# Performance work log

Measured on AMD Instinct MI355X. Metric: run time of the kernel, lower is better.

Reference implementation:

```python
import jax, jax.numpy as jnp
import numpy as np

MAX_SHIFT = 2
SMOOTH = 1.0

def setup_inputs() -> dict:
    key = jax.random.key(0)
    k1, k2 = jax.random.split(key)
    # predicted probabilities in [0,1)
    inputs = jax.random.uniform(k1, (64, 1, 512, 512), dtype=jnp.float32)
    # soft targets (the original accepts any float mask); uniform works as a stand-in
    targets = jax.random.uniform(k2, (64, 1, 512, 512), dtype=jnp.float32)
    return {"inputs": inputs, "targets": targets}

def reference(inputs, targets):
    # all (shift_y, shift_x) pairs from the 5x5 nested loop
    shifts = jnp.array(
        [(sy, sx)
         for sx in range(-MAX_SHIFT, MAX_SHIFT + 1)
         for sy in range(-MAX_SHIFT, MAX_SHIFT + 1)],
        dtype=jnp.int32,
    )  # [25, 2]

    # global sums; targets.sum() is invariant under roll but kept per the original math
    i_sum = inputs.sum()
    t_sum = targets.sum()

    def dice_loss(shift):
        st = jnp.roll(targets, (shift[0], shift[1]), axis=(2, 3))
        intersection = jnp.sum(inputs * st)
        return 1.0 - (2.0 * intersection + SMOOTH) / (i_sum + t_sum + SMOOTH)

    losses = jax.vmap(dice_loss)(shifts)  # [25]
    return jnp.min(losses)
```

## Files before the change

### kernel.cpp

```cpp
#include <hip/hip_runtime.h>

#define H 512
#define W 512
#define RROWS 32
#define TGR  (RROWS + 4)
#define NCHUNK (TGR * 2)

__device__ __forceinline__ float wave_sum_dpp(float x) {
#define DPP_STEP(ctrl)                                                          \
    x += __int_as_float(__builtin_amdgcn_update_dpp(                            \
        0, __float_as_int(x), (ctrl), 0xF, 0xF, true))
    DPP_STEP(0x111);
    DPP_STEP(0x112);
    DPP_STEP(0x114);
    DPP_STEP(0x118);
    DPP_STEP(0x142);
    DPP_STEP(0x143);
#undef DPP_STEP
    return x;
}

__device__ __forceinline__ float4 ld4(const float* p) {
    return *reinterpret_cast<const float4*>(p);
}
__device__ __forceinline__ float2 ld2(const float* p) {
    return *reinterpret_cast<const float2*>(p);
}

__device__ __forceinline__ void gl_lds16(const float* g, float* l) {
    __builtin_amdgcn_global_load_lds(
        (const __attribute__((address_space(1))) void*)g,
        (__attribute__((address_space(3))) void*)l,
        16, 0, 0);
}

__global__ __launch_bounds__(512, 4)
void dice_partial(const float* __restrict__ in, const float* __restrict__ tg,
                  float* __restrict__ ws, int nblocks) {
    __shared__ __align__(16) float tgs[TGR * W];
    __shared__ float warr[8][32];

    const int tid  = threadIdx.x;
    const int wave = tid >> 6, lane = tid & 63;

    const int bid = blockIdx.x;
    const int wrk = (bid & 7) * (nblocks >> 3) + (bid >> 3);

    const int b  = wrk >> 4;
    const int y0 = (wrk & 15) * RROWS;
    const float* __restrict__ ib = in + (size_t)b * (H * W);
    const float* __restrict__ tb = tg + (size_t)b * (H * W);

    const int c0 = lane * 8;

    const int ry = y0 + wave * 4;
    float4 ia[4], ic[4];
#pragma unroll
    for (int yi = 0; yi < 4; ++yi) {
        const float* rp = ib + (size_t)(ry + yi) * W;
        ia[yi] = ld4(rp + c0);
        ic[yi] = ld4(rp + c0 + 4);
    }

#pragma unroll
    for (int k = 0; k < 9; ++k) {
        const int c    = wave * 9 + k;
        const int rr   = c >> 1;
        const int half = (c & 1) * 256;
        const int ra   = (y0 - 2 + rr) & (H - 1);
        gl_lds16(tb + (size_t)ra * W + half + lane * 4, &tgs[c * 256]);
    }

    float iv[4][8];
    float isum = 0.f;
#pragma unroll
    for (int yi = 0; yi < 4; ++yi) {
        iv[yi][0] = ia[yi].x; iv[yi][1] = ia[yi].y;
        iv[yi][2] = ia[yi].z; iv[yi][3] = ia[yi].w;
        iv[yi][4] = ic[yi].x; iv[yi][5] = ic[yi].y;
        iv[yi][6] = ic[yi].z; iv[yi][7] = ic[yi].w;
#pragma unroll
        for (int j = 0; j < 8; ++j) isum += iv[yi][j];
    }
    isum = wave_sum_dpp(isum);
    if (lane == 63) warr[wave][25] = isum;

    __syncthreads();

    float acc[25];
#pragma unroll
    for (int k = 0; k < 25; ++k) acc[k] = 0.f;
    float tsum = 0.f;

#pragma unroll
    for (int t = 0; t < 8; ++t) {
        const float* rowp = &tgs[(wave * 4 + t) * W];
        float tw[12];
        const float4 a  = ld4(rowp + c0);
        const float4 cc = ld4(rowp + c0 + 4);
        const float2 lf = ld2(rowp + ((c0 - 2) & (W - 1)));
        const float2 rg = ld2(rowp + ((c0 + 8) & (W - 1)));
        tw[0]  = lf.x; tw[1]  = lf.y;
        tw[2]  = a.x;  tw[3]  = a.y;  tw[4] = a.z;  tw[5] = a.w;
        tw[6]  = cc.x; tw[7]  = cc.y; tw[8] = cc.z; tw[9] = cc.w;
        tw[10] = rg.x; tw[11] = rg.y;

        if (t >= 2 && t <= 5) {
#pragma unroll
            for (int j = 0; j < 8; ++j) tsum += tw[j + 2];
        }

#pragma unroll
        for (int yi = 0; yi < 4; ++yi) {
            const int sy = yi + 2 - t;
            if (sy < -2 || sy > 2) continue;
#pragma unroll
            for (int sx = -2; sx <= 2; ++sx) {
#pragma unroll
                for (int j = 0; j < 8; ++j)
                    acc[(sy + 2) * 5 + (sx + 2)] += iv[yi][j] * tw[j + 2 - sx];
            }
        }
    }

#pragma unroll
    for (int k = 0; k < 25; ++k) {
        const float v = wave_sum_dpp(acc[k]);
        if (lane == 63) warr[wave][k] = v;
    }
    {
        const float u = wave_sum_dpp(tsum);
        if (lane == 63) warr[wave][26] = u;
    }

    __syncthreads();
    if (tid < 27) {
        float s = 0.f;
#pragma unroll
        for (int w = 0; w < 8; ++w) s += warr[w][tid];
        ws[tid * nblocks + bid] = s;
    }
}

__global__ __launch_bounds__(256)
void dice_reduce(const float* __restrict__ ws, float* __restrict__ tot, int nblocks) {
    __shared__ float red[4];
    const int k = blockIdx.x;
    const int tid = threadIdx.x;
    const float* p = ws + (size_t)k * nblocks;

    float s = 0.f;
    for (int i = tid; i < nblocks; i += 256) s += p[i];
    s = wave_sum_dpp(s);
    if ((tid & 63) == 63) red[tid >> 6] = s;
    __syncthreads();
    if (tid == 0) tot[k] = red[0] + red[1] + red[2] + red[3];
}

__global__ void dice_out(const float* __restrict__ tot, float* __restrict__ out) {
    const int tid = threadIdx.x;
    float v = (tid < 25) ? tot[tid] : -1e30f;
#pragma unroll
    for (int off = 32; off; off >>= 1) v = fmaxf(v, __shfl_down(v, off, 64));
    if (tid == 0) {
        const float denom = tot[25] + tot[26] + 1.0f;
        out[0] = 1.0f - (2.0f * v + 1.0f) / denom;
    }
}

extern "C" void kernel_launch(void* const* d_in, const int* in_sizes, int n_in,
                              void* d_out, int out_size, void* d_ws, size_t ws_size,
                              hipStream_t stream) {
    const float* inputs  = (const float*)d_in[0];
    const float* targets = (const float*)d_in[1];
    float* out = (float*)d_out;
    float* ws  = (float*)d_ws;

    const int B = in_sizes[0] / (H * W);
    const int nblocks = B * (H / RROWS);

    float* tot = ws + (size_t)27 * nblocks;

    dice_partial<<<nblocks, 512, 0, stream>>>(inputs, targets, ws, nblocks);
    dice_reduce<<<27, 256, 0, stream>>>(ws, tot, nblocks);
    dice_out<<<1, 64, 0, stream>>>(tot, out);
}
```

Before: 38.76 us.

## Double-buffer slabs of inputs and targets in LDS with async loads

Each block now handles 64 rows of one image, split into 8 slabs of 8 rows. For each slab, both the input rows and the haloed target rows are staged into double-buffered LDS with global_load_lds, and the next slab's load is issued while the current one is computed. This overlaps memory traffic with the 25-shift correlation work, and the target halo is reloaded once per 8 rows instead of once per 32. The cost is more halo re-reads of targets, smaller 256-thread blocks, a barrier per slab, and only 512 blocks in the grid, which may lower parallelism and occupancy.

```diff
diff --git a/kernel.cpp b/kernel.cpp
--- a/kernel.cpp
+++ b/kernel.cpp
@@ -2,9 +2,10 @@
 
 #define H 512
 #define W 512
-#define RROWS 32
-#define TGR  (RROWS + 4)
-#define NCHUNK (TGR * 2)
+#define SLAB 8
+#define TROWS 12
+#define BROWS 20
+#define NSLAB 8
 
 __device__ __forceinline__ float wave_sum_dpp(float x) {
 #define DPP_STEP(ctrl)                                                          \
@@ -34,11 +35,10 @@
         16, 0, 0);
 }
 
-__global__ __launch_bounds__(512, 4)
+__global__ __launch_bounds__(256)
 void dice_partial(const float* __restrict__ in, const float* __restrict__ tg,
                   float* __restrict__ ws, int nblocks) {
-    __shared__ __align__(16) float tgs[TGR * W];
-    __shared__ float warr[8][32];
+    __shared__ __align__(16) float buf[2][BROWS][W];
 
     const int tid  = threadIdx.x;
     const int wave = tid >> 6, lane = tid & 63;
@@ -46,98 +46,103 @@
     const int bid = blockIdx.x;
     const int wrk = (bid & 7) * (nblocks >> 3) + (bid >> 3);
 
-    const int b  = wrk >> 4;
-    const int y0 = (wrk & 15) * RROWS;
-    const float* __restrict__ ib = in + (size_t)b * (H * W);
-    const float* __restrict__ tb = tg + (size_t)b * (H * W);
+    const int b   = wrk >> 3;
+    const int r0  = (wrk & 7) * 64;
+    const float* __restrict__ inb = in + (size_t)b * (H * W);
+    const float* __restrict__ tgb = tg + (size_t)b * (H * W);
 
     const int c0 = lane * 8;
 
-    const int ry = y0 + wave * 4;
-    float4 ia[4], ic[4];
-#pragma unroll
-    for (int yi = 0; yi < 4; ++yi) {
-        const float* rp = ib + (size_t)(ry + yi) * W;
-        ia[yi] = ld4(rp + c0);
-        ic[yi] = ld4(rp + c0 + 4);
+#define STAGE(s, sb) {                                                          \
+        const int y0s = r0 + (s) * SLAB;                                        \
+        _Pragma("unroll")                                                       \
+        for (int k = 0; k < 10; ++k) {                                          \
+            const int e    = wave * 10 + k;                                     \
+            const int rr   = e >> 1;                                            \
+            const int half = (e & 1) * 256;                                     \
+            const float* src = (rr < TROWS)                                     \
+                ? tgb + (size_t)((y0s - 2 + rr) & (H - 1)) * W + half           \
+                : inb + (size_t)(y0s + (rr - TROWS)) * W + half;                \
+            gl_lds16(src + lane * 4, &buf[sb][rr][half]);                       \
+        }                                                                       \
     }
-
-#pragma unroll
-    for (int k = 0; k < 9; ++k) {
-        const int c    = wave * 9 + k;
-        const int rr   = c >> 1;
-        const int half = (c & 1) * 256;
-        const int ra   = (y0 - 2 + rr) & (H - 1);
-        gl_lds16(tb + (size_t)ra * W + half + lane * 4, &tgs[c * 256]);
-    }
-
-    float iv[4][8];
-    float isum = 0.f;
-#pragma unroll
-    for (int yi = 0; yi < 4; ++yi) {
-        iv[yi][0] = ia[yi].x; iv[yi][1] = ia[yi].y;
-        iv[yi][2] = ia[yi].z; iv[yi][3] = ia[yi].w;
-        iv[yi][4] = ic[yi].x; iv[yi][5] = ic[yi].y;
-        iv[yi][6] = ic[yi].z; iv[yi][7] = ic[yi].w;
-#pragma unroll
-        for (int j = 0; j < 8; ++j) isum += iv[yi][j];
-    }
-    isum = wave_sum_dpp(isum);
-    if (lane == 63) warr[wave][25] = isum;
-
-    __syncthreads();
 
     float acc[25];
 #pragma unroll
     for (int k = 0; k < 25; ++k) acc[k] = 0.f;
-    float tsum = 0.f;
+    float isum = 0.f, tsum = 0.f;
+
+    STAGE(0, 0)
+    __syncthreads();
 
 #pragma unroll
-    for (int t = 0; t < 8; ++t) {
-        const float* rowp = &tgs[(wave * 4 + t) * W];
-        float tw[12];
-        const float4 a  = ld4(rowp + c0);
-        const float4 cc = ld4(rowp + c0 + 4);
-        const float2 lf = ld2(rowp + ((c0 - 2) & (W - 1)));
-        const float2 rg = ld2(rowp + ((c0 + 8) & (W - 1)));
-        tw[0]  = lf.x; tw[1]  = lf.y;
-        tw[2]  = a.x;  tw[3]  = a.y;  tw[4] = a.z;  tw[5] = a.w;
-        tw[6]  = cc.x; tw[7]  = cc.y; tw[8] = cc.z; tw[9] = cc.w;
-        tw[10] = rg.x; tw[11] = rg.y;
+    for (int s = 0; s < NSLAB; ++s) {
+        if (s + 1 < NSLAB) STAGE(s + 1, (s + 1) & 1)
 
-        if (t >= 2 && t <= 5) {
+        const int sb = s & 1;
+        float iv[2][8];
 #pragma unroll
-            for (int j = 0; j < 8; ++j) tsum += tw[j + 2];
+        for (int yi = 0; yi < 2; ++yi) {
+            const float* rowp = &buf[sb][TROWS + 2 * wave + yi][0];
+            const float4 a  = ld4(rowp + c0);
+            const float4 cc = ld4(rowp + c0 + 4);
+            iv[yi][0] = a.x;  iv[yi][1] = a.y;  iv[yi][2] = a.z;  iv[yi][3] = a.w;
+            iv[yi][4] = cc.x; iv[yi][5] = cc.y; iv[yi][6] = cc.z; iv[yi][7] = cc.w;
+#pragma unroll
+            for (int j = 0; j < 8; ++j) isum += iv[yi][j];
         }
 
 #pragma unroll
-        for (int yi = 0; yi < 4; ++yi) {
-            const int sy = yi + 2 - t;
-            if (sy < -2 || sy > 2) continue;
+        for (int t = 0; t < 6; ++t) {
+            const float* rowp = &buf[sb][2 * wave + t][0];
+            float tw[12];
+            const float4 a  = ld4(rowp + c0);
+            const float4 cc = ld4(rowp + c0 + 4);
+            const float2 lf = ld2(rowp + ((c0 - 2) & (W - 1)));
+            const float2 rg = ld2(rowp + ((c0 + 8) & (W - 1)));
+            tw[0]  = lf.x; tw[1]  = lf.y;
+            tw[2]  = a.x;  tw[3]  = a.y;  tw[4] = a.z;  tw[5] = a.w;
+            tw[6]  = cc.x; tw[7]  = cc.y; tw[8] = cc.z; tw[9] = cc.w;
+            tw[10] = rg.x; tw[11] = rg.y;
+
+            if (t == 2 || t == 3) {
 #pragma unroll
-            for (int sx = -2; sx <= 2; ++sx) {
+                for (int j = 0; j < 8; ++j) tsum += tw[j + 2];
+            }
+
 #pragma unroll
-                for (int j = 0; j < 8; ++j)
-                    acc[(sy + 2) * 5 + (sx + 2)] += iv[yi][j] * tw[j + 2 - sx];
+            for (int yi = 0; yi < 2; ++yi) {
+                const int sy = yi + 2 - t;
+                if (sy < -2 || sy > 2) continue;
+#pragma unroll
+                for (int sx = -2; sx <= 2; ++sx) {
+#pragma unroll
+                    for (int j = 0; j < 8; ++j)
+                        acc[(sy + 2) * 5 + (sx + 2)] += iv[yi][j] * tw[j + 2 - sx];
+                }
             }
         }
+
+        __syncthreads();
     }
+#undef STAGE
 
+    float* warrf = &buf[0][0][0];
 #pragma unroll
     for (int k = 0; k < 25; ++k) {
         const float v = wave_sum_dpp(acc[k]);
-        if (lane == 63) warr[wave][k] = v;
+        if (lane == 63) warrf[wave * 32 + k] = v;
     }
     {
+        const float v = wave_sum_dpp(isum);
+        if (lane == 63) warrf[wave * 32 + 25] = v;
         const float u = wave_sum_dpp(tsum);
-        if (lane == 63) warr[wave][26] = u;
+        if (lane == 63) warrf[wave * 32 + 26] = u;
     }
 
     __syncthreads();
     if (tid < 27) {
-        float s = 0.f;
-#pragma unroll
-        for (int w = 0; w < 8; ++w) s += warr[w][tid];
+        const float s = warrf[tid] + warrf[32 + tid] + warrf[64 + tid] + warrf[96 + tid];
         ws[tid * nblocks + bid] = s;
     }
 }
@@ -177,11 +182,11 @@
     float* ws  = (float*)d_ws;
 
     const int B = in_sizes[0] / (H * W);
-    const int nblocks = B * (H / RROWS);
+    const int nblocks = B * 8;
 
     float* tot = ws + (size_t)27 * nblocks;
 
-    dice_partial<<<nblocks, 512, 0, stream>>>(inputs, targets, ws, nblocks);
+    dice_partial<<<nblocks, 256, 0, stream>>>(inputs, targets, ws, nblocks);
     dice_reduce<<<27, 256, 0, stream>>>(ws, tot, nblocks);
     dice_out<<<1, 64, 0, stream>>>(tot, out);
 }
```

New measurement: 146.8 us. +278.7%, slower.

## Process four row slabs per block with double-buffered LDS target staging

Applied to the files above, without the earlier changes.

Each block now handles four 32-row slabs instead of one, and stages the next slab's target rows into a second LDS buffer while computing on the current one. This overlaps global-to-LDS loads with the FMA work and cuts the block count by four, which reduces per-block setup and the number of partials to reduce. In exchange it doubles LDS use per block (two 36x512 float buffers), lowers occupancy (launch bounds go from 4 to 2), and adds a barrier per slab.

```diff
diff --git a/kernel.cpp b/kernel.cpp
--- a/kernel.cpp
+++ b/kernel.cpp
@@ -2,9 +2,10 @@
 
 #define H 512
 #define W 512
-#define RROWS 32
-#define TGR  (RROWS + 4)
-#define NCHUNK (TGR * 2)
+#define SLAB 32
+#define TGR  36
+#define NSLAB 4
+#define NWAVE 8
 
 __device__ __forceinline__ float wave_sum_dpp(float x) {
 #define DPP_STEP(ctrl)                                                          \
@@ -34,94 +35,105 @@
         16, 0, 0);
 }
 
-__global__ __launch_bounds__(512, 4)
+__global__ __launch_bounds__(512, 2)
 void dice_partial(const float* __restrict__ in, const float* __restrict__ tg,
                   float* __restrict__ ws, int nblocks) {
-    __shared__ __align__(16) float tgs[TGR * W];
-    __shared__ float warr[8][32];
+    __shared__ __align__(16) float buf[2][TGR * W];
+    __shared__ float warr[NWAVE][32];
 
     const int tid  = threadIdx.x;
     const int wave = tid >> 6, lane = tid & 63;
 
     const int bid = blockIdx.x;
     const int wrk = (bid & 7) * (nblocks >> 3) + (bid >> 3);
-
-    const int b  = wrk >> 4;
-    const int y0 = (wrk & 15) * RROWS;
-    const float* __restrict__ ib = in + (size_t)b * (H * W);
-    const float* __restrict__ tb = tg + (size_t)b * (H * W);
+    const int b   = wrk >> 2;
+    const int r0  = (wrk & 3) * (NSLAB * SLAB);
+    const float* __restrict__ inb = in + (size_t)b * (H * W);
+    const float* __restrict__ tgb = tg + (size_t)b * (H * W);
 
     const int c0 = lane * 8;
 
-    const int ry = y0 + wave * 4;
-    float4 ia[4], ic[4];
-#pragma unroll
-    for (int yi = 0; yi < 4; ++yi) {
-        const float* rp = ib + (size_t)(ry + yi) * W;
-        ia[yi] = ld4(rp + c0);
-        ic[yi] = ld4(rp + c0 + 4);
-    }
-
-#pragma unroll
-    for (int k = 0; k < 9; ++k) {
-        const int c    = wave * 9 + k;
-        const int rr   = c >> 1;
-        const int half = (c & 1) * 256;
-        const int ra   = (y0 - 2 + rr) & (H - 1);
-        gl_lds16(tb + (size_t)ra * W + half + lane * 4, &tgs[c * 256]);
-    }
-
-    float iv[4][8];
-    float isum = 0.f;
-#pragma unroll
-    for (int yi = 0; yi < 4; ++yi) {
-        iv[yi][0] = ia[yi].x; iv[yi][1] = ia[yi].y;
-        iv[yi][2] = ia[yi].z; iv[yi][3] = ia[yi].w;
-        iv[yi][4] = ic[yi].x; iv[yi][5] = ic[yi].y;
-        iv[yi][6] = ic[yi].z; iv[yi][7] = ic[yi].w;
-#pragma unroll
-        for (int j = 0; j < 8; ++j) isum += iv[yi][j];
-    }
-    isum = wave_sum_dpp(isum);
-    if (lane == 63) warr[wave][25] = isum;
-
+#define STAGE(s, sb) {                                                          \
+        const int y0s = r0 + (s) * SLAB;                                        \
+        _Pragma("unroll")                                                       \
+        for (int k = 0; k < 9; ++k) {                                           \
+            const int c    = wave * 9 + k;                                      \
+            const int rr   = c >> 1;                                            \
+            const int half = (c & 1) * 256;                                     \
+            gl_lds16(tgb + (size_t)((y0s - 2 + rr) & (H - 1)) * W + half        \
+                         + lane * 4,                                            \
+                     &buf[sb][rr * W + half]);                                  \
+        }                                                                       \
+    }
+
+    float acc[25];
+#pragma unroll
+    for (int k = 0; k < 25; ++k) acc[k] = 0.f;
+    float isum = 0.f, tsum = 0.f;
+
+    STAGE(0, 0)
     __syncthreads();
 
-    float acc[25];
-#pragma unroll
-    for (int k = 0; k < 25; ++k) acc[k] = 0.f;
-    float tsum = 0.f;
-
-#pragma unroll
-    for (int t = 0; t < 8; ++t) {
-        const float* rowp = &tgs[(wave * 4 + t) * W];
-        float tw[12];
-        const float4 a  = ld4(rowp + c0);
-        const float4 cc = ld4(rowp + c0 + 4);
-        const float2 lf = ld2(rowp + ((c0 - 2) & (W - 1)));
-        const float2 rg = ld2(rowp + ((c0 + 8) & (W - 1)));
-        tw[0]  = lf.x; tw[1]  = lf.y;
-        tw[2]  = a.x;  tw[3]  = a.y;  tw[4] = a.z;  tw[5] = a.w;
-        tw[6]  = cc.x; tw[7]  = cc.y; tw[8] = cc.z; tw[9] = cc.w;
-        tw[10] = rg.x; tw[11] = rg.y;
-
-        if (t >= 2 && t <= 5) {
-#pragma unroll
-            for (int j = 0; j < 8; ++j) tsum += tw[j + 2];
+#pragma unroll 1
+    for (int s = 0; s < NSLAB; ++s) {
+        const int sb = s & 1;
+        const int ry = r0 + s * SLAB + wave * 4;
+
+        float4 ia[4], ic[4];
+#pragma unroll
+        for (int yi = 0; yi < 4; ++yi) {
+            const float* rp = inb + (size_t)(ry + yi) * W;
+            ia[yi] = ld4(rp + c0);
+            ic[yi] = ld4(rp + c0 + 4);
         }
 
+        if (s + 1 < NSLAB) STAGE(s + 1, sb ^ 1)
+
+        float iv[4][8];
 #pragma unroll
         for (int yi = 0; yi < 4; ++yi) {
-            const int sy = yi + 2 - t;
-            if (sy < -2 || sy > 2) continue;
-#pragma unroll
-            for (int sx = -2; sx <= 2; ++sx) {
-#pragma unroll
-                for (int j = 0; j < 8; ++j)
-                    acc[(sy + 2) * 5 + (sx + 2)] += iv[yi][j] * tw[j + 2 - sx];
+            iv[yi][0] = ia[yi].x; iv[yi][1] = ia[yi].y;
+            iv[yi][2] = ia[yi].z; iv[yi][3] = ia[yi].w;
+            iv[yi][4] = ic[yi].x; iv[yi][5] = ic[yi].y;
+            iv[yi][6] = ic[yi].z; iv[yi][7] = ic[yi].w;
+#pragma unroll
+            for (int j = 0; j < 8; ++j) isum += iv[yi][j];
+        }
+
+#pragma unroll
+        for (int t = 0; t < 8; ++t) {
+            const float* rowp = &buf[sb][(wave * 4 + t) * W];
+            float tw[12];
+            const float4 a  = ld4(rowp + c0);
+            const float4 cc = ld4(rowp + c0 + 4);
+            const float2 lf = ld2(rowp + ((c0 - 2) & (W - 1)));
+            const float2 rg = ld2(rowp + ((c0 + 8) & (W - 1)));
+            tw[0]  = lf.x; tw[1]  = lf.y;
+            tw[2]  = a.x;  tw[3]  = a.y;  tw[4] = a.z;  tw[5] = a.w;
+            tw[6]  = cc.x; tw[7]  = cc.y; tw[8] = cc.z; tw[9] = cc.w;
+            tw[10] = rg.x; tw[11] = rg.y;
+
+            if (t >= 2 && t <= 5) {
+#pragma unroll
+                for (int j = 0; j < 8; ++j) tsum += tw[j + 2];
+            }
+
+#pragma unroll
+            for (int yi = 0; yi < 4; ++yi) {
+                const int sy = yi + 2 - t;
+                if (sy < -2 || sy > 2) continue;
+#pragma unroll
+                for (int sx = -2; sx <= 2; ++sx) {
+#pragma unroll
+                    for (int j = 0; j < 8; ++j)
+                        acc[(sy + 2) * 5 + (sx + 2)] += iv[yi][j] * tw[j + 2 - sx];
+                }
             }
         }
-    }
+
+        __syncthreads();
+    }
+#undef STAGE
 
 #pragma unroll
     for (int k = 0; k < 25; ++k) {
@@ -129,6 +141,8 @@
         if (lane == 63) warr[wave][k] = v;
     }
     {
+        const float v = wave_sum_dpp(isum);
+        if (lane == 63) warr[wave][25] = v;
         const float u = wave_sum_dpp(tsum);
         if (lane == 63) warr[wave][26] = u;
     }
@@ -137,7 +151,7 @@
     if (tid < 27) {
         float s = 0.f;
 #pragma unroll
-        for (int w = 0; w < 8; ++w) s += warr[w][tid];
+        for (int w = 0; w < NWAVE; ++w) s += warr[w][tid];
         ws[tid * nblocks + bid] = s;
     }
 }
@@ -177,7 +191,7 @@
     float* ws  = (float*)d_ws;
 
     const int B = in_sizes[0] / (H * W);
-    const int nblocks = B * (H / RROWS);
+    const int nblocks = B * 4;
 
     float* tot = ws + (size_t)27 * nblocks;
 
```

New measurement: 54.98 us. +41.9%, slower.
